# Optimization experiments

Hardware: AMD Instinct MI355X
Metric: run time of the kernel (lower is better)

The kernel has to match this reference:

```python
import jax, jax.numpy as jnp
import numpy as np

NUM_HEADS = 16


def setup_inputs() -> dict:
    key = jax.random.key(0)
    k1, k2, k3 = jax.random.split(key, 3)
    B, N, C = 8, 16384, 128  # window_size == dim == 128, N = ws*ws
    x = jax.random.normal(k1, (B, N, C), dtype=jnp.float32)
    w_qkv = jax.random.normal(k2, (3 * C, C), dtype=jnp.float32) * (C ** -0.5)
    b_qkv = jax.random.normal(k3, (3 * C,), dtype=jnp.float32) * 0.01
    return {"x": x, "w_qkv": w_qkv, "b_qkv": b_qkv}


def reference(x, w_qkv, b_qkv):
    B, N, C = x.shape
    ws = C  # the Linear over the last axis forces window_size == dim
    H = NUM_HEADS
    scale = (C // H) ** -0.5  # torch code scales by (dim//num_heads)**-0.5
    # [B,N,C] -> [B,ws,ws,C] -> [B,C,ws,ws]
    x4 = jnp.transpose(x.reshape(B, ws, ws, C), (0, 3, 1, 2))
    # Linear over last axis (length ws == dim): [B,C,ws,3C]
    qkv = jnp.einsum('bcwd,ed->bcwe', x4, w_qkv) + b_qkv
    # reshape(B,C,3,H,-1).permute(2,0,3,1,4) -> [3,B,H,C, ws*C/H]
    qkv = jnp.transpose(qkv.reshape(B, C, 3, H, -1), (2, 0, 3, 1, 4))
    q, k, v = qkv[0], qkv[1], qkv[2]  # each [B,H,C,D] with D = ws*C/H
    attn = jax.nn.softmax(jnp.einsum('bhcd,bhed->bhce', q, k) * scale, axis=-1)  # [B,H,C,C]
    out = jnp.einsum('bhce,bhed->bhcd', attn, v)  # [B,H,C,D]
    # transpose(1,2).reshape(B,C,ws,ws).permute(0,2,3,1).view(B,N,C)
    out = jnp.transpose(out, (0, 2, 1, 3)).reshape(B, C, ws, ws)
    out = jnp.transpose(out, (0, 2, 3, 1)).reshape(B, N, C)
    return out
```

## Files before the change

### kernel.cpp

```cpp
#include <hip/hip_runtime.h>
#include <hip/hip_bf16.h>
#include <stdint.h>


#define B_ 8
#define N_ 16384
#define C_ 128
#define H_ 16
#define E3 384
#define DH 1024

typedef float f32x4 __attribute__((ext_vector_type(4)));
typedef _Float16 f16x8 __attribute__((ext_vector_type(8)));
typedef unsigned short u16x8 __attribute__((ext_vector_type(8)));
typedef unsigned short u16x4 __attribute__((ext_vector_type(4)));

#define MFMA16(a, b, c) __builtin_amdgcn_mfma_f32_16x16x32_f16((a), (b), (c), 0, 0, 0)

__device__ __forceinline__ unsigned short f2h(float f) {
  union { _Float16 h; unsigned short u; } x;
  x.h = (_Float16)f;
  return x.u;
}

__global__ __launch_bounds__(256) void convert_w_kernel(const float* __restrict__ wq,
                                                        unsigned short* __restrict__ wh) {
  int i = blockIdx.x * 256 + threadIdx.x;
  float4 v = ((const float4*)wq)[i];
  u16x4 o;
  o[0] = f2h(v.x); o[1] = f2h(v.y); o[2] = f2h(v.z); o[3] = f2h(v.w);
  ((u16x4*)wh)[i] = o;
}

__global__ __launch_bounds__(256) void qkv_proj_kernel(
    const float* __restrict__ x,
    const float* __restrict__ wq,
    const unsigned short* __restrict__ wh,
    const float* __restrict__ bq,
    unsigned short* __restrict__ qk2,
    unsigned short* __restrict__ vT2) {
  const int w = blockIdx.x & 127;
  const int half = blockIdx.x >> 7;
  const int b = blockIdx.y;
  const int t = threadIdx.x;
  const int l = t & 63;
  const int wv = t >> 6;

  __shared__ __align__(16) unsigned short xt[128 * 128];
  char* xtb = (char*)xt;

  const float* xg = x + ((size_t)(b * N_ + w * 128)) * C_;
#pragma unroll
  for (int it = 0; it < 2; ++it) {
    int task = t + it * 256;
    int c0 = (task & 31) * 4;
    int d0 = (task >> 5) * 8;
    u16x8 pk0, pk1, pk2, pk3;
#pragma unroll
    for (int j = 0; j < 8; ++j) {
      float4 v = *(const float4*)(xg + (d0 + j) * C_ + c0);
      pk0[j] = f2h(v.x);
      pk1[j] = f2h(v.y);
      pk2[j] = f2h(v.z);
      pk3[j] = f2h(v.w);
    }
    *(u16x8*)(xtb + c0 * 256 + ((d0 * 2) ^ ((c0 & 7) << 4))) = pk0;
    *(u16x8*)(xtb + (c0 + 1) * 256 + ((d0 * 2) ^ (((c0 + 1) & 7) << 4))) = pk1;
    *(u16x8*)(xtb + (c0 + 2) * 256 + ((d0 * 2) ^ (((c0 + 2) & 7) << 4))) = pk2;
    *(u16x8*)(xtb + (c0 + 3) * 256 + ((d0 * 2) ^ (((c0 + 3) & 7) << 4))) = pk3;
  }
  __syncthreads();

  const int c00 = (wv & 1) * 64;
  const int ehalf = (wv >> 1) * 32;

  f16x8 ax[4][4];
#pragma unroll
  for (int mf = 0; mf < 4; ++mf)
#pragma unroll
    for (int ks = 0; ks < 4; ++ks) {
      int cl = c00 + mf * 16 + (l & 15);
      ax[mf][ks] = *(const f16x8*)(xtb + cl * 256 + (((ks * 64) + ((l >> 4) * 16)) ^ ((cl & 7) << 4)));
    }

  const f32x4 fzero = {0.f, 0.f, 0.f, 0.f};
  const bool useWh = (wh != nullptr);

#pragma unroll
  for (int es = 0; es < 3; ++es) {
    const int esub = half * 3 + es;
    const int e00 = esub * 64 + ehalf;
    const int f00 = w * E3 + e00;
    const int type = f00 >> 14;

    f16x8 bw[2][4];
#pragma unroll
    for (int nf = 0; nf < 2; ++nf)
#pragma unroll
      for (int ks = 0; ks < 4; ++ks) {
        int e = e00 + nf * 16 + (l & 15);
        if (useWh) {
          bw[nf][ks] = *(const f16x8*)(wh + e * 128 + ks * 32 + ((l >> 4) * 8));
        } else {
          const float* wp = wq + e * 128 + ks * 32 + ((l >> 4) * 8);
          float4 w0 = *(const float4*)(wp);
          float4 w1 = *(const float4*)(wp + 4);
          f16x8 bb;
          bb[0] = (_Float16)w0.x; bb[1] = (_Float16)w0.y;
          bb[2] = (_Float16)w0.z; bb[3] = (_Float16)w0.w;
          bb[4] = (_Float16)w1.x; bb[5] = (_Float16)w1.y;
          bb[6] = (_Float16)w1.z; bb[7] = (_Float16)w1.w;
          bw[nf][ks] = bb;
        }
      }

    f32x4 acc[4][2];
#pragma unroll
    for (int mf = 0; mf < 4; ++mf)
#pragma unroll
      for (int nf = 0; nf < 2; ++nf) acc[mf][nf] = fzero;

    if (type < 2) {
#pragma unroll
      for (int ks = 0; ks < 4; ++ks)
#pragma unroll
        for (int mf = 0; mf < 4; ++mf)
#pragma unroll
          for (int nf = 0; nf < 2; ++nf)
            acc[mf][nf] = MFMA16(bw[nf][ks], ax[mf][ks], acc[mf][nf]);
#pragma unroll
      for (int nf = 0; nf < 2; ++nf) {
        int ft = (f00 + nf * 16) >> 4;
        float4 bb = *(const float4*)(bq + e00 + nf * 16 + ((l >> 4) * 4));
#pragma unroll
        for (int mf = 0; mf < 4; ++mf) {
          int cb = (c00 >> 4) + mf;
          size_t tb = (((size_t)b * 2048 + ft) * 8 + cb) * 256;
          u16x4 ov;
          ov[0] = f2h(acc[mf][nf][0] + bb.x);
          ov[1] = f2h(acc[mf][nf][1] + bb.y);
          ov[2] = f2h(acc[mf][nf][2] + bb.z);
          ov[3] = f2h(acc[mf][nf][3] + bb.w);
          *(u16x4*)(qk2 + tb + l * 4) = ov;
        }
      }
    } else {
#pragma unroll
      for (int ks = 0; ks < 4; ++ks)
#pragma unroll
        for (int mf = 0; mf < 4; ++mf)
#pragma unroll
          for (int nf = 0; nf < 2; ++nf)
            acc[mf][nf] = MFMA16(ax[mf][ks], bw[nf][ks], acc[mf][nf]);
#pragma unroll
      for (int nf = 0; nf < 2; ++nf) {
        int fnf = f00 + nf * 16;
        int hh = (fnf >> 10) & 15;
        int ddt = (fnf & 1023) >> 4;
        float bias = bq[e00 + nf * 16 + (l & 15)];
#pragma unroll
        for (int mf = 0; mf < 4; ++mf) {
          int cb = (c00 >> 4) + mf;
          size_t tb = ((((size_t)b * 16 + hh) * 64 + ddt) * 8 + cb) * 256;
          u16x4 ov;
#pragma unroll
          for (int r = 0; r < 4; ++r) ov[r] = f2h(acc[mf][nf][r] + bias);
          *(u16x4*)(vT2 + tb + l * 4) = ov;
        }
      }
    }
  }
}

__global__ __launch_bounds__(256) void attn_kernel(
    const unsigned short* __restrict__ qk2,
    const unsigned short* __restrict__ vT2,
    float* __restrict__ out) {
  const int bid = blockIdx.x;
  const int ch = bid >> 7;
  const int bh = bid & 127;
  const int b = bh >> 4;
  const int h = bh & 15;
  const int t = threadIdx.x;
  const int l = t & 63;
  const int wv = t >> 6;

  __shared__ __align__(16) char smem[8192 + 32768 + 2048];
  char* QS = smem;
  char* KS = smem + 8192;
  float* RED = (float*)(smem + 40960);

  const f32x4 fzero = {0.f, 0.f, 0.f, 0.f};
  f32x4 acc[2][2];
#pragma unroll
  for (int mf = 0; mf < 2; ++mf)
#pragma unroll
    for (int nf = 0; nf < 2; ++nf) acc[mf][nf] = fzero;

  const int e0w = wv * 32;

  uint4 qv[2], kv[8];
  {
    const int ft0q = h * 64;
    const int ft0k = 1024 + h * 64;
#pragma unroll
    for (int i = 0; i < 2; ++i) {
      int idx = t + i * 256;
      int ftl = idx >> 6, cbl = (idx >> 5) & 1, m = idx & 31;
      qv[i] = *(const uint4*)(qk2 + (((size_t)b * 2048 + ft0q + ftl) * 8 + ch * 2 + cbl) * 256 + m * 8);
    }
#pragma unroll
    for (int i = 0; i < 8; ++i) {
      int idx = t + i * 256;
      int ftl = idx >> 8, cb = (idx >> 5) & 7, m = idx & 31;
      kv[i] = *(const uint4*)(qk2 + (((size_t)b * 2048 + ft0k + ftl) * 8 + cb) * 256 + m * 8);
    }
  }

  for (int dc = 0; dc < 8; ++dc) {
    if (dc) __syncthreads();
#pragma unroll
    for (int i = 0; i < 2; ++i) {
      int idx = t + i * 256;
      int ftl = idx >> 6, cbl = (idx >> 5) & 1, m = idx & 31;
      int row0 = cbl * 16 + (m & 7) * 2;
      int fb = ftl * 32 + (m >> 3) * 8;
      uint4 v = qv[i];
      *(uint2*)(QS + row0 * 256 + (fb ^ ((row0 & 7) << 4))) = make_uint2(v.x, v.y);
      *(uint2*)(QS + (row0 + 1) * 256 + (fb ^ (((row0 + 1) & 7) << 4))) = make_uint2(v.z, v.w);
    }
#pragma unroll
    for (int i = 0; i < 8; ++i) {
      int idx = t + i * 256;
      int ftl = idx >> 8, cb = (idx >> 5) & 7, m = idx & 31;
      int row0 = cb * 16 + (m & 7) * 2;
      int fb = ftl * 32 + (m >> 3) * 8;
      uint4 v = kv[i];
      *(uint2*)(KS + row0 * 256 + (fb ^ ((row0 & 7) << 4))) = make_uint2(v.x, v.y);
      *(uint2*)(KS + (row0 + 1) * 256 + (fb ^ (((row0 + 1) & 7) << 4))) = make_uint2(v.z, v.w);
    }
    __syncthreads();

    if (dc < 7) {
      const int ft0q = h * 64 + (dc + 1) * 8;
      const int ft0k = 1024 + h * 64 + (dc + 1) * 8;
#pragma unroll
      for (int i = 0; i < 2; ++i) {
        int idx = t + i * 256;
        int ftl = idx >> 6, cbl = (idx >> 5) & 1, m = idx & 31;
        qv[i] = *(const uint4*)(qk2 + (((size_t)b * 2048 + ft0q + ftl) * 8 + ch * 2 + cbl) * 256 + m * 8);
      }
#pragma unroll
      for (int i = 0; i < 8; ++i) {
        int idx = t + i * 256;
        int ftl = idx >> 8, cb = (idx >> 5) & 7, m = idx & 31;
        kv[i] = *(const uint4*)(qk2 + (((size_t)b * 2048 + ft0k + ftl) * 8 + cb) * 256 + m * 8);
      }
    }

#pragma unroll
    for (int ks = 0; ks < 4; ++ks) {
      f16x8 aQ[2], bK[2];
#pragma unroll
      for (int mf = 0; mf < 2; ++mf) {
        int cl = mf * 16 + (l & 15);
        aQ[mf] = *(const f16x8*)(QS + cl * 256 + (((ks * 64) + ((l >> 4) * 16)) ^ ((cl & 7) << 4)));
      }
#pragma unroll
      for (int nf = 0; nf < 2; ++nf) {
        int el = e0w + nf * 16 + (l & 15);
        bK[nf] = *(const f16x8*)(KS + el * 256 + (((ks * 64) + ((l >> 4) * 16)) ^ ((el & 7) << 4)));
      }
#pragma unroll
      for (int mf = 0; mf < 2; ++mf)
#pragma unroll
        for (int nf = 0; nf < 2; ++nf)
          acc[mf][nf] = MFMA16(aQ[mf], bK[nf], acc[mf][nf]);
    }
  }

  uint4 vv[8];
#pragma unroll
  for (int i = 0; i < 8; ++i) {
    int idx = t + i * 256;
    int ddtl = idx >> 8, cb = (idx >> 5) & 7, m = idx & 31;
    vv[i] = *(const uint4*)(vT2 + ((((size_t)(b * 16 + h)) * 64 + ddtl) * 8 + cb) * 256 + m * 8);
  }

  const float SC = 0.35355339059327f * 1.44269504088896f;
  float mrow[2][4];
#pragma unroll
  for (int mf = 0; mf < 2; ++mf)
#pragma unroll
    for (int r = 0; r < 4; ++r) {
      float mx = fmaxf(acc[mf][0][r], acc[mf][1][r]);
      mx = fmaxf(mx, __shfl_xor(mx, 1));
      mx = fmaxf(mx, __shfl_xor(mx, 2));
      mx = fmaxf(mx, __shfl_xor(mx, 4));
      mx = fmaxf(mx, __shfl_xor(mx, 8));
      int cl = mf * 16 + ((l >> 4) * 4) + r;
      if ((l & 15) == 0) RED[cl * 4 + wv] = mx;
    }
  __syncthreads();
#pragma unroll
  for (int mf = 0; mf < 2; ++mf)
#pragma unroll
    for (int r = 0; r < 4; ++r) {
      int cl = mf * 16 + ((l >> 4) * 4) + r;
      float4 v = *(const float4*)(RED + cl * 4);
      mrow[mf][r] = fmaxf(fmaxf(v.x, v.y), fmaxf(v.z, v.w));
    }
#pragma unroll
  for (int mf = 0; mf < 2; ++mf)
#pragma unroll
    for (int r = 0; r < 4; ++r) {
      float s0 = 0.f;
#pragma unroll
      for (int nf = 0; nf < 2; ++nf) {
        float p = exp2f((acc[mf][nf][r] - mrow[mf][r]) * SC);
        acc[mf][nf][r] = p;
        s0 += p;
      }
      s0 += __shfl_xor(s0, 1);
      s0 += __shfl_xor(s0, 2);
      s0 += __shfl_xor(s0, 4);
      s0 += __shfl_xor(s0, 8);
      int cl = mf * 16 + ((l >> 4) * 4) + r;
      if ((l & 15) == 0) RED[256 + cl * 4 + wv] = s0;
    }
#pragma unroll
  for (int mf = 0; mf < 2; ++mf)
#pragma unroll
    for (int nf = 0; nf < 2; ++nf)
#pragma unroll
      for (int r = 0; r < 4; ++r) {
        int cl = mf * 16 + ((l >> 4) * 4) + r;
        int el = e0w + nf * 16 + (l & 15);
        *(unsigned short*)(QS + cl * 256 + ((el * 2) ^ ((cl & 7) << 4))) = f2h(acc[mf][nf][r]);
      }
  __syncthreads();
  float invc[2];
#pragma unroll
  for (int mf = 0; mf < 2; ++mf) {
    int cl = mf * 16 + (l & 15);
    float4 v = *(const float4*)(RED + 256 + cl * 4);
    invc[mf] = 1.f / (v.x + v.y + v.z + v.w);
  }

  for (int dc2 = 0; dc2 < 8; ++dc2) {
    if (dc2) __syncthreads();
#pragma unroll
    for (int i = 0; i < 8; ++i) {
      int idx = t + i * 256;
      int ddtl = idx >> 8, cb = (idx >> 5) & 7, m = idx & 31;
      int row0 = ddtl * 16 + (m & 7) * 2;
      int cbyte = cb * 32 + (m >> 3) * 8;
      uint4 v = vv[i];
      *(uint2*)(KS + row0 * 256 + (cbyte ^ ((row0 & 7) << 4))) = make_uint2(v.x, v.y);
      *(uint2*)(KS + (row0 + 1) * 256 + (cbyte ^ (((row0 + 1) & 7) << 4))) = make_uint2(v.z, v.w);
    }
    __syncthreads();

    if (dc2 < 7) {
#pragma unroll
      for (int i = 0; i < 8; ++i) {
        int idx = t + i * 256;
        int ddtl = idx >> 8, cb = (idx >> 5) & 7, m = idx & 31;
        vv[i] = *(const uint4*)(vT2 + ((((size_t)(b * 16 + h)) * 64 + (dc2 + 1) * 8 + ddtl) * 8 + cb) * 256 + m * 8);
      }
    }

    f32x4 acc2[2][2];
#pragma unroll
    for (int nf = 0; nf < 2; ++nf)
#pragma unroll
      for (int mf = 0; mf < 2; ++mf) acc2[nf][mf] = fzero;

#pragma unroll
    for (int ks = 0; ks < 4; ++ks) {
      f16x8 aP[2], bV[2];
#pragma unroll
      for (int mf = 0; mf < 2; ++mf) {
        int cl = mf * 16 + (l & 15);
        aP[mf] = *(const f16x8*)(QS + cl * 256 + (((ks * 64) + ((l >> 4) * 16)) ^ ((cl & 7) << 4)));
      }
#pragma unroll
      for (int nf = 0; nf < 2; ++nf) {
        int dl = e0w + nf * 16 + (l & 15);
        bV[nf] = *(const f16x8*)(KS + dl * 256 + (((ks * 64) + ((l >> 4) * 16)) ^ ((dl & 7) << 4)));
      }
#pragma unroll
      for (int nf = 0; nf < 2; ++nf)
#pragma unroll
        for (int mf = 0; mf < 2; ++mf)
          acc2[nf][mf] = MFMA16(bV[nf], aP[mf], acc2[nf][mf]);
    }

#pragma unroll
    for (int nf = 0; nf < 2; ++nf)
#pragma unroll
      for (int mf = 0; mf < 2; ++mf) {
        int c = ch * 32 + mf * 16 + (l & 15);
#pragma unroll
        for (int r = 0; r < 4; ++r) {
          int d = dc2 * 128 + e0w + nf * 16 + ((l >> 4) * 4) + r;
          out[((size_t)(b * N_ + h * DH + d)) * C_ + c] = acc2[nf][mf][r] * invc[mf];
        }
      }
  }
}

extern "C" void kernel_launch(void* const* d_in, const int* in_sizes, int n_in,
                              void* d_out, int out_size, void* d_ws, size_t ws_size,
                              hipStream_t stream) {
  const float* x = (const float*)d_in[0];
  const float* wq = (const float*)d_in[1];
  const float* bq = (const float*)d_in[2];
  unsigned short* qk2 = (unsigned short*)d_ws;
  unsigned short* vT2 = qk2 + 33554432UL;
  unsigned short* wh = vT2 + 16777216UL;

  const size_t baseNeed = (33554432UL + 16777216UL) * 2;
  if (ws_size < baseNeed) return;
  const bool useWh = ws_size >= baseNeed + 49152UL * 2;

  if (useWh) convert_w_kernel<<<48, 256, 0, stream>>>(wq, wh);
  qkv_proj_kernel<<<dim3(256, 8), 256, 0, stream>>>(x, wq, useWh ? wh : nullptr, bq, qk2, vT2);
  attn_kernel<<<512, 256, 0, stream>>>(qk2, vT2, (float*)d_out);
}
```

Baseline: 85.49 us.

## Fuse Q projection into attention kernel, project only K and V beforehand

The projection kernel now computes only the K and V parts (skipping windows that produce only Q), and writes K into a smaller buffer. The attention kernel loads the needed x slices, converts them to fp16 in shared memory, and computes each Q chunk with MFMA directly into shared memory before the QK^T product. This removes the Q write and read round trip through global memory and shrinks the workspace. In exchange it adds projection work, weight loads and an extra barrier inside the attention loop.

```diff
diff --git a/kernel.cpp b/kernel.cpp
--- a/kernel.cpp
+++ b/kernel.cpp
@@ -32,15 +32,15 @@
   ((u16x4*)wh)[i] = o;
 }
 
-__global__ __launch_bounds__(256) void qkv_proj_kernel(
+__global__ __launch_bounds__(256) void kv_proj_kernel(
     const float* __restrict__ x,
     const float* __restrict__ wq,
     const unsigned short* __restrict__ wh,
     const float* __restrict__ bq,
-    unsigned short* __restrict__ qk2,
+    unsigned short* __restrict__ kv2,
     unsigned short* __restrict__ vT2) {
-  const int w = blockIdx.x & 127;
-  const int half = blockIdx.x >> 7;
+  const int w = 42 + (blockIdx.x % 86);
+  const int half = blockIdx.x / 86;
   const int b = blockIdx.y;
   const int t = threadIdx.x;
   const int l = t & 63;
@@ -92,6 +92,7 @@
     const int e00 = esub * 64 + ehalf;
     const int f00 = w * E3 + e00;
     const int type = f00 >> 14;
+    if (type == 0) continue;
 
     f16x8 bw[2][4];
 #pragma unroll
@@ -120,7 +121,7 @@
 #pragma unroll
       for (int nf = 0; nf < 2; ++nf) acc[mf][nf] = fzero;
 
-    if (type < 2) {
+    if (type == 1) {
 #pragma unroll
       for (int ks = 0; ks < 4; ++ks)
 #pragma unroll
@@ -130,18 +131,18 @@
             acc[mf][nf] = MFMA16(bw[nf][ks], ax[mf][ks], acc[mf][nf]);
 #pragma unroll
       for (int nf = 0; nf < 2; ++nf) {
-        int ft = (f00 + nf * 16) >> 4;
+        int ft = ((f00 + nf * 16) >> 4) - 1024;
         float4 bb = *(const float4*)(bq + e00 + nf * 16 + ((l >> 4) * 4));
 #pragma unroll
         for (int mf = 0; mf < 4; ++mf) {
           int cb = (c00 >> 4) + mf;
-          size_t tb = (((size_t)b * 2048 + ft) * 8 + cb) * 256;
+          size_t tb = (((size_t)b * 1024 + ft) * 8 + cb) * 256;
           u16x4 ov;
           ov[0] = f2h(acc[mf][nf][0] + bb.x);
           ov[1] = f2h(acc[mf][nf][1] + bb.y);
           ov[2] = f2h(acc[mf][nf][2] + bb.z);
           ov[3] = f2h(acc[mf][nf][3] + bb.w);
-          *(u16x4*)(qk2 + tb + l * 4) = ov;
+          *(u16x4*)(kv2 + tb + l * 4) = ov;
         }
       }
     } else {
@@ -173,7 +174,11 @@
 }
 
 __global__ __launch_bounds__(256) void attn_kernel(
-    const unsigned short* __restrict__ qk2,
+    const float* __restrict__ x,
+    const float* __restrict__ wq,
+    const unsigned short* __restrict__ wh,
+    const float* __restrict__ bq,
+    const unsigned short* __restrict__ kv2,
     const unsigned short* __restrict__ vT2,
     float* __restrict__ out) {
   const int bid = blockIdx.x;
@@ -184,11 +189,13 @@
   const int t = threadIdx.x;
   const int l = t & 63;
   const int wv = t >> 6;
-
-  __shared__ __align__(16) char smem[8192 + 32768 + 2048];
-  char* QS = smem;
-  char* KS = smem + 8192;
-  float* RED = (float*)(smem + 40960);
+  const bool useWh = (wh != nullptr);
+
+  __shared__ __align__(16) char smem[8192 + 8192 + 32768 + 2048];
+  char* XS = smem;
+  char* QS = smem + 8192;
+  char* KS = smem + 16384;
+  float* RED = (float*)(smem + 49152);
 
   const f32x4 fzero = {0.f, 0.f, 0.f, 0.f};
   f32x4 acc[2][2];
@@ -198,37 +205,30 @@
     for (int nf = 0; nf < 2; ++nf) acc[mf][nf] = fzero;
 
   const int e0w = wv * 32;
-
-  uint4 qv[2], kv[8];
+  const int cq = t & 7;
+  const int dg = t >> 3;
+
+  uint4 kv[8];
+  float4 xv[4];
   {
-    const int ft0q = h * 64;
-    const int ft0k = 1024 + h * 64;
-#pragma unroll
-    for (int i = 0; i < 2; ++i) {
-      int idx = t + i * 256;
-      int ftl = idx >> 6, cbl = (idx >> 5) & 1, m = idx & 31;
-      qv[i] = *(const uint4*)(qk2 + (((size_t)b * 2048 + ft0q + ftl) * 8 + ch * 2 + cbl) * 256 + m * 8);
-    }
+    const int ft0k = h * 64;
 #pragma unroll
     for (int i = 0; i < 8; ++i) {
       int idx = t + i * 256;
       int ftl = idx >> 8, cb = (idx >> 5) & 7, m = idx & 31;
-      kv[i] = *(const uint4*)(qk2 + (((size_t)b * 2048 + ft0k + ftl) * 8 + cb) * 256 + m * 8);
-    }
+      kv[i] = *(const uint4*)(kv2 + (((size_t)b * 1024 + ft0k + ftl) * 8 + cb) * 256 + m * 8);
+    }
+    const int k0 = 8 * h;
+    const int w0 = k0 / 3;
+    const float* xgq = x + ((size_t)(b * N_ + w0 * 128 + dg * 4)) * C_ + ch * 32 + cq * 4;
+#pragma unroll
+    for (int j = 0; j < 4; ++j) xv[j] = *(const float4*)(xgq + (size_t)j * C_);
   }
 
   for (int dc = 0; dc < 8; ++dc) {
+    const int kk = 8 * h + dc;
+    const int e0c = (kk % 3) * 128;
     if (dc) __syncthreads();
-#pragma unroll
-    for (int i = 0; i < 2; ++i) {
-      int idx = t + i * 256;
-      int ftl = idx >> 6, cbl = (idx >> 5) & 1, m = idx & 31;
-      int row0 = cbl * 16 + (m & 7) * 2;
-      int fb = ftl * 32 + (m >> 3) * 8;
-      uint4 v = qv[i];
-      *(uint2*)(QS + row0 * 256 + (fb ^ ((row0 & 7) << 4))) = make_uint2(v.x, v.y);
-      *(uint2*)(QS + (row0 + 1) * 256 + (fb ^ (((row0 + 1) & 7) << 4))) = make_uint2(v.z, v.w);
-    }
 #pragma unroll
     for (int i = 0; i < 8; ++i) {
       int idx = t + i * 256;
@@ -239,24 +239,89 @@
       *(uint2*)(KS + row0 * 256 + (fb ^ ((row0 & 7) << 4))) = make_uint2(v.x, v.y);
       *(uint2*)(KS + (row0 + 1) * 256 + (fb ^ (((row0 + 1) & 7) << 4))) = make_uint2(v.z, v.w);
     }
+    {
+      int d0b = dg * 8;
+#pragma unroll
+      for (int ci = 0; ci < 4; ++ci) {
+        int c = cq * 4 + ci;
+        u16x4 ov;
+        ov[0] = f2h(xv[0][ci]); ov[1] = f2h(xv[1][ci]);
+        ov[2] = f2h(xv[2][ci]); ov[3] = f2h(xv[3][ci]);
+        *(u16x4*)(XS + c * 256 + (d0b ^ ((c & 7) << 4))) = ov;
+      }
+    }
     __syncthreads();
 
     if (dc < 7) {
-      const int ft0q = h * 64 + (dc + 1) * 8;
-      const int ft0k = 1024 + h * 64 + (dc + 1) * 8;
-#pragma unroll
-      for (int i = 0; i < 2; ++i) {
-        int idx = t + i * 256;
-        int ftl = idx >> 6, cbl = (idx >> 5) & 1, m = idx & 31;
-        qv[i] = *(const uint4*)(qk2 + (((size_t)b * 2048 + ft0q + ftl) * 8 + ch * 2 + cbl) * 256 + m * 8);
-      }
+      const int ft0k = h * 64 + (dc + 1) * 8;
 #pragma unroll
       for (int i = 0; i < 8; ++i) {
         int idx = t + i * 256;
         int ftl = idx >> 8, cb = (idx >> 5) & 7, m = idx & 31;
-        kv[i] = *(const uint4*)(qk2 + (((size_t)b * 2048 + ft0k + ftl) * 8 + cb) * 256 + m * 8);
-      }
-    }
+        kv[i] = *(const uint4*)(kv2 + (((size_t)b * 1024 + ft0k + ftl) * 8 + cb) * 256 + m * 8);
+      }
+      const int kn = kk + 1;
+      const int wn = kn / 3;
+      const float* xgq = x + ((size_t)(b * N_ + wn * 128 + dg * 4)) * C_ + ch * 32 + cq * 4;
+#pragma unroll
+      for (int j = 0; j < 4; ++j) xv[j] = *(const float4*)(xgq + (size_t)j * C_);
+    }
+
+    {
+      f16x8 bw[2][4];
+      const int ew = e0c + wv * 32;
+#pragma unroll
+      for (int nf = 0; nf < 2; ++nf)
+#pragma unroll
+        for (int ks = 0; ks < 4; ++ks) {
+          int e = ew + nf * 16 + (l & 15);
+          if (useWh) {
+            bw[nf][ks] = *(const f16x8*)(wh + e * 128 + ks * 32 + ((l >> 4) * 8));
+          } else {
+            const float* wp = wq + e * 128 + ks * 32 + ((l >> 4) * 8);
+            float4 w0 = *(const float4*)(wp);
+            float4 w1 = *(const float4*)(wp + 4);
+            f16x8 bb;
+            bb[0] = (_Float16)w0.x; bb[1] = (_Float16)w0.y;
+            bb[2] = (_Float16)w0.z; bb[3] = (_Float16)w0.w;
+            bb[4] = (_Float16)w1.x; bb[5] = (_Float16)w1.y;
+            bb[6] = (_Float16)w1.z; bb[7] = (_Float16)w1.w;
+            bw[nf][ks] = bb;
+          }
+        }
+      f32x4 qacc[2][2];
+#pragma unroll
+      for (int mf = 0; mf < 2; ++mf)
+#pragma unroll
+        for (int nf = 0; nf < 2; ++nf) qacc[mf][nf] = fzero;
+#pragma unroll
+      for (int ks = 0; ks < 4; ++ks) {
+        f16x8 axq[2];
+#pragma unroll
+        for (int mf = 0; mf < 2; ++mf) {
+          int cl = mf * 16 + (l & 15);
+          axq[mf] = *(const f16x8*)(XS + cl * 256 + (((ks * 64) + ((l >> 4) * 16)) ^ ((cl & 7) << 4)));
+        }
+#pragma unroll
+        for (int mf = 0; mf < 2; ++mf)
+#pragma unroll
+          for (int nf = 0; nf < 2; ++nf)
+            qacc[mf][nf] = MFMA16(axq[mf], bw[nf][ks], qacc[mf][nf]);
+      }
+#pragma unroll
+      for (int nf = 0; nf < 2; ++nf) {
+        float bias = bq[ew + nf * 16 + (l & 15)];
+        int fl = wv * 32 + nf * 16 + (l & 15);
+#pragma unroll
+        for (int mf = 0; mf < 2; ++mf)
+#pragma unroll
+          for (int r = 0; r < 4; ++r) {
+            int cl = mf * 16 + ((l >> 4) * 4) + r;
+            *(unsigned short*)(QS + cl * 256 + ((fl * 2) ^ ((cl & 7) << 4))) = f2h(qacc[mf][nf][r] + bias);
+          }
+      }
+    }
+    __syncthreads();
 
 #pragma unroll
     for (int ks = 0; ks < 4; ++ks) {
@@ -416,15 +481,15 @@
   const float* x = (const float*)d_in[0];
   const float* wq = (const float*)d_in[1];
   const float* bq = (const float*)d_in[2];
-  unsigned short* qk2 = (unsigned short*)d_ws;
-  unsigned short* vT2 = qk2 + 33554432UL;
+  unsigned short* kv2 = (unsigned short*)d_ws;
+  unsigned short* vT2 = kv2 + 16777216UL;
   unsigned short* wh = vT2 + 16777216UL;
 
-  const size_t baseNeed = (33554432UL + 16777216UL) * 2;
+  const size_t baseNeed = (16777216UL + 16777216UL) * 2;
   if (ws_size < baseNeed) return;
   const bool useWh = ws_size >= baseNeed + 49152UL * 2;
 
   if (useWh) convert_w_kernel<<<48, 256, 0, stream>>>(wq, wh);
-  qkv_proj_kernel<<<dim3(256, 8), 256, 0, stream>>>(x, wq, useWh ? wh : nullptr, bq, qk2, vT2);
-  attn_kernel<<<512, 256, 0, stream>>>(qk2, vT2, (float*)d_out);
+  kv_proj_kernel<<<dim3(172, 8), 256, 0, stream>>>(x, wq, useWh ? wh : nullptr, bq, kv2, vT2);
+  attn_kernel<<<512, 256, 0, stream>>>(x, wq, useWh ? wh : nullptr, bq, kv2, vT2, (float*)d_out);
 }
```

After: 99.74 us. +16.7%, slower.
